# Performance work log

Measured on AMD Instinct MI355X. Metric: run time of the kernel, lower is better.

## Reference

```python
import jax, jax.numpy as jnp
import numpy as np

ENC_DIM = 512
QUERY_DIM = 1024
ATTN_DIM = 128
CONV_CH = 32
KERNEL = 31
B, T = 64, 2048


def setup_inputs() -> dict:
    key = jax.random.key(0)
    ks = jax.random.split(key, 9)
    s = 0.02
    encoder_outputs = jax.random.normal(ks[0], (B, T, ENC_DIM), dtype=jnp.float32)
    decoder_hidden = jax.random.normal(ks[1], (B, QUERY_DIM), dtype=jnp.float32)
    prev_attention = jax.random.uniform(ks[2], (B, T), dtype=jnp.float32)
    prev_attention = prev_attention / jnp.sum(prev_attention, axis=1, keepdims=True)
    Wq = jax.random.normal(ks[3], (QUERY_DIM, ATTN_DIM), dtype=jnp.float32) * s
    Wk = jax.random.normal(ks[4], (ENC_DIM, ATTN_DIM), dtype=jnp.float32) * s
    conv_w = jax.random.normal(ks[5], (CONV_CH, 1, KERNEL), dtype=jnp.float32) * s  # OIH
    conv_b = jax.random.normal(ks[6], (CONV_CH,), dtype=jnp.float32) * s
    Wloc = jax.random.normal(ks[7], (CONV_CH, ATTN_DIM), dtype=jnp.float32) * s
    v = jax.random.normal(ks[8], (ATTN_DIM,), dtype=jnp.float32) * s
    return {"encoder_outputs": encoder_outputs, "decoder_hidden": decoder_hidden,
            "prev_attention": prev_attention, "Wq": Wq, "Wk": Wk,
            "conv_w": conv_w, "conv_b": conv_b, "Wloc": Wloc, "v": v}


def reference(encoder_outputs, decoder_hidden, prev_attention, Wq, Wk, conv_w, conv_b, Wloc, v):
    # query: [B, 1, A]
    query = (decoder_hidden @ Wq)[:, None, :]
    # keys: [B, T, A]
    keys = jnp.einsum('bte,ea->bta', encoder_outputs, Wk)
    # location conv: prev_attention [B, T] -> [B, 1, T] -> [B, C, T], SAME padding
    pad = (KERNEL - 1) // 2
    loc = jax.lax.conv_general_dilated(
        prev_attention[:, None, :], conv_w,
        window_strides=(1,), padding=[(pad, pad)],
        dimension_numbers=('NCH', 'OIH', 'NCH'))
    loc = loc + conv_b[None, :, None]
    # [B, T, C] -> [B, T, A]
    location_term = jnp.einsum('bct,ca->bta', loc, Wloc)
    energy = jnp.einsum('bta,a->bt', jnp.tanh(keys + query + location_term), v)
    return jax.nn.softmax(energy, axis=1)
```

## Files before the change

### kernel.cpp

```cpp
#include <hip/hip_runtime.h>
#include <hip/hip_bf16.h>

#define B_  64
#define T_  2048
#define E_  512
#define Q_  1024
#define A_  128
#define C_  32
#define KW_ 31

using bf16x8 = __attribute__((ext_vector_type(8))) short;
using f32x4  = __attribute__((ext_vector_type(4))) float;

__device__ __forceinline__ short f2bf(float f) {
  union { float f; unsigned u; } x; x.f = f;
  unsigned r = x.u + 0x7fffu + ((x.u >> 16) & 1u);
  return (short)(r >> 16);
}

__device__ __forceinline__ bf16x8 pack8(float4 a, float4 b) {
  union { bf16x8 v; __hip_bfloat162 h[4]; } u;
  u.h[0] = __float22bfloat162_rn(make_float2(a.x, a.y));
  u.h[1] = __float22bfloat162_rn(make_float2(a.z, a.w));
  u.h[2] = __float22bfloat162_rn(make_float2(b.x, b.y));
  u.h[3] = __float22bfloat162_rn(make_float2(b.z, b.w));
  return u.v;
}

__device__ __forceinline__ float fast_tanh(float x) {
  float e2 = __expf(2.f * x);
  return 1.f - 2.f * __builtin_amdgcn_rcpf(e2 + 1.f);
}

__device__ __forceinline__ void gload16(const void* g, void* l) {
  __builtin_amdgcn_global_load_lds(
      (const __attribute__((address_space(1))) unsigned int*)g,
      (__attribute__((address_space(3))) unsigned int*)l, 16, 0, 0);
}

__global__ __launch_bounds__(256) void prep_kernel(
    const float* __restrict__ dh, const float* __restrict__ Wq,
    const float* __restrict__ conv_b, const float* __restrict__ Wloc,
    const float* __restrict__ Wk, const float* __restrict__ conv_w,
    unsigned short* __restrict__ wkf, float* __restrict__ q2p)
{
  int blk = blockIdx.x;
  int tid = threadIdx.x;
  if (blk < 512) {
    __shared__ float part[128];
    int b = blk >> 3, kq = blk & 7;
    int a = tid & 127, kh = tid >> 7;
    const float* dhr = dh + b * Q_ + kq * 128 + kh * 64;
    const float* wq  = Wq + (size_t)(kq * 128 + kh * 64) * A_ + a;
    float s = 0.f;
    #pragma unroll 8
    for (int k = 0; k < 64; ++k) s += dhr[k] * wq[(size_t)k * A_];
    if (kh) part[a] = s;
    __syncthreads();
    if (!kh) {
      s += part[a];
      if (kq == 0) {
        float t = 0.f;
        for (int c = 0; c < C_; ++c) t += conv_b[c] * Wloc[c * A_ + a];
        s += t;
      }
      q2p[(kq * B_ + b) * A_ + a] = s;
    }
  } else if (blk < 544) {
    int wave = tid >> 6, lane = tid & 63;
    int g = (blk - 512) * 4 + wave;
    int ks = g >> 3, nt = g & 7;
    int lg = lane >> 4, lr = lane & 15;
    bf16x8 o;
    #pragma unroll
    for (int j = 0; j < 8; ++j)
      o[j] = f2bf(Wk[(ks * 32 + lg * 8 + j) * A_ + nt * 16 + lr]);
    *(bf16x8*)(wkf + ((size_t)g * 64 + lane) * 8) = o;
  } else {
    __shared__ float G[32][128];
    for (int i = tid; i < 4096; i += 256) {
      int j = i >> 7, a = i & 127;
      float s = 0.f;
      if (j < KW_)
        for (int c = 0; c < C_; ++c) s += conv_w[c * KW_ + j] * Wloc[c * A_ + a];
      G[j][a] = s;
    }
    __syncthreads();
    int wave = tid >> 6, lane = tid & 63;
    int lg = lane >> 4, lr = lane & 15;
    #pragma unroll
    for (int h = 0; h < 2; ++h) {
      int nt = wave * 2 + h;
      bf16x8 o;
      #pragma unroll
      for (int j = 0; j < 8; ++j) o[j] = f2bf(G[lg * 8 + j][nt * 16 + lr]);
      *(bf16x8*)(wkf + ((size_t)(128 + nt) * 64 + lane) * 8) = o;
    }
  }
}

__global__ __launch_bounds__(512, 2) void energy_kernel(
    const float* __restrict__ enc, const float* __restrict__ prev,
    const unsigned short* __restrict__ wkfall,
    const float* __restrict__ q2p, const float* __restrict__ vvec,
    float* __restrict__ outexp, float* __restrict__ psum)
{
  __shared__ unsigned short sWB[69632];
  __shared__ float swsum[8];

  int tid = threadIdx.x;
  int wave = tid >> 6, lane = tid & 63;
  int lg = lane >> 4, lr = lane & 15;
  int m0 = blockIdx.x * 512;
  int b  = m0 >> 11;
  int wm = m0 + wave * 64;

  #pragma unroll
  for (int s = 0; s < 17; ++s)
    gload16(wkfall + (size_t)s * 4096 + wave * 512 + lane * 8,
            &sWB[s * 4096 + wave * 512]);

  const float* prevb = prev + b * T_;
  int tl = (m0 & (T_ - 1)) + wave * 64 + lr;
  float pv[32];
  #pragma unroll
  for (int g = 0; g < 4; ++g) {
    #pragma unroll
    for (int j = 0; j < 8; ++j) {
      int u = tl + 16 * g - 15 + lg * 8 + j;
      int uc = min(max(u, 0), T_ - 1);
      pv[g * 8 + j] = prevb[uc];
    }
  }

  const float* eR = enc + (size_t)(wm + lr) * E_ + lg * 8;
  float4 sA[8], sB[8];
  #pragma unroll
  for (int g = 0; g < 4; ++g) {
    const float* rg = eR + (size_t)g * 16 * E_;
    sA[2 * g]     = *(const float4*)(rg);
    sA[2 * g + 1] = *(const float4*)(rg + 4);
    sB[2 * g]     = *(const float4*)(rg + 32);
    sB[2 * g + 1] = *(const float4*)(rg + 36);
  }

  asm volatile("s_waitcnt vmcnt(0)" ::: "memory");
  __builtin_amdgcn_sched_barrier(0);
  __builtin_amdgcn_s_barrier();

  f32x4 acc[4][8];
  {
    bf16x8 ap[4];
    #pragma unroll
    for (int g = 0; g < 4; ++g) {
      float m[8];
      #pragma unroll
      for (int j = 0; j < 8; ++j) {
        int u = tl + 16 * g - 15 + lg * 8 + j;
        m[j] = ((unsigned)u < (unsigned)T_) ? pv[g * 8 + j] : 0.f;
      }
      ap[g] = pack8(make_float4(m[0], m[1], m[2], m[3]),
                    make_float4(m[4], m[5], m[6], m[7]));
    }
    const unsigned short* base = &sWB[16 * 4096 + lane * 8];
    #pragma unroll
    for (int nt = 0; nt < 8; ++nt) {
      bf16x8 bfr = *(const bf16x8*)(base + nt * 512);
      #pragma unroll
      for (int g = 0; g < 4; ++g)
        acc[g][nt] = __builtin_amdgcn_mfma_f32_16x16x32_bf16(ap[g], bfr, (f32x4){0,0,0,0}, 0, 0, 0);
    }
  }

  #pragma unroll 1
  for (int i = 0; i < 8; ++i) {
    {
      bf16x8 af[4];
      #pragma unroll
      for (int g = 0; g < 4; ++g) af[g] = pack8(sA[2 * g], sA[2 * g + 1]);
      if (i < 7) {
        #pragma unroll
        for (int g = 0; g < 4; ++g) {
          const float* rg = eR + (size_t)g * 16 * E_ + (2 * i + 2) * 32;
          sA[2 * g]     = *(const float4*)(rg);
          sA[2 * g + 1] = *(const float4*)(rg + 4);
        }
      }
      const unsigned short* base = &sWB[(2 * i) * 4096 + lane * 8];
      #pragma unroll
      for (int nt = 0; nt < 8; ++nt) {
        bf16x8 bfr = *(const bf16x8*)(base + nt * 512);
        #pragma unroll
        for (int g = 0; g < 4; ++g)
          acc[g][nt] = __builtin_amdgcn_mfma_f32_16x16x32_bf16(af[g], bfr, acc[g][nt], 0, 0, 0);
      }
    }
    {
      bf16x8 af[4];
      #pragma unroll
      for (int g = 0; g < 4; ++g) af[g] = pack8(sB[2 * g], sB[2 * g + 1]);
      if (i < 7) {
        #pragma unroll
        for (int g = 0; g < 4; ++g) {
          const float* rg = eR + (size_t)g * 16 * E_ + (2 * i + 3) * 32;
          sB[2 * g]     = *(const float4*)(rg);
          sB[2 * g + 1] = *(const float4*)(rg + 4);
        }
      }
      const unsigned short* base = &sWB[(2 * i + 1) * 4096 + lane * 8];
      #pragma unroll
      for (int nt = 0; nt < 8; ++nt) {
        bf16x8 bfr = *(const bf16x8*)(base + nt * 512);
        #pragma unroll
        for (int g = 0; g < 4; ++g)
          acc[g][nt] = __builtin_amdgcn_mfma_f32_16x16x32_bf16(af[g], bfr, acc[g][nt], 0, 0, 0);
      }
    }
  }

  float qv[8], vv[8];
  #pragma unroll
  for (int nt = 0; nt < 8; ++nt) {
    int n = nt * 16 + lr;
    float s = 0.f;
    #pragma unroll
    for (int p = 0; p < 8; ++p) s += q2p[(p * B_ + b) * A_ + n];
    qv[nt] = s;
    vv[nt] = vvec[n];
  }
  float ssum = 0.f;
  #pragma unroll
  for (int g = 0; g < 4; ++g) {
    float p0 = 0, p1 = 0, p2 = 0, p3 = 0;
    #pragma unroll
    for (int nt = 0; nt < 8; ++nt) {
      p0 += fast_tanh(acc[g][nt][0] + qv[nt]) * vv[nt];
      p1 += fast_tanh(acc[g][nt][1] + qv[nt]) * vv[nt];
      p2 += fast_tanh(acc[g][nt][2] + qv[nt]) * vv[nt];
      p3 += fast_tanh(acc[g][nt][3] + qv[nt]) * vv[nt];
    }
    #pragma unroll
    for (int off = 1; off < 16; off <<= 1) {
      p0 += __shfl_xor(p0, off, 64);
      p1 += __shfl_xor(p1, off, 64);
      p2 += __shfl_xor(p2, off, 64);
      p3 += __shfl_xor(p3, off, 64);
    }
    float e0 = __expf(p0), e1 = __expf(p1), e2 = __expf(p2), e3 = __expf(p3);
    ssum += (e0 + e1) + (e2 + e3);
    if (lr == 0)
      *(float4*)(outexp + wm + g * 16 + lg * 4) = make_float4(e0, e1, e2, e3);
  }
  ssum += __shfl_xor(ssum, 16, 64);
  ssum += __shfl_xor(ssum, 32, 64);
  if (lane == 0) swsum[wave] = ssum;
  __syncthreads();
  if (tid == 0) {
    float s = 0.f;
    #pragma unroll
    for (int wv = 0; wv < 8; ++wv) s += swsum[wv];
    psum[b * 4 + (blockIdx.x & 3)] = s;
  }
}

__global__ __launch_bounds__(256) void norm_kernel(float* __restrict__ out,
                                                   const float* __restrict__ psum)
{
  int b = blockIdx.x, tid = threadIdx.x;
  float s = 0.f;
  #pragma unroll
  for (int p = 0; p < 4; ++p) s += psum[b * 4 + p];
  float inv = 1.f / s;
  float4* row = (float4*)(out + (size_t)b * T_);
  #pragma unroll
  for (int j = 0; j < 2; ++j) {
    float4 x = row[tid + j * 256];
    x.x *= inv; x.y *= inv; x.z *= inv; x.w *= inv;
    row[tid + j * 256] = x;
  }
}

extern "C" void kernel_launch(void* const* d_in, const int* in_sizes, int n_in,
                              void* d_out, int out_size, void* d_ws, size_t ws_size,
                              hipStream_t stream)
{
  const float* enc   = (const float*)d_in[0];
  const float* dh    = (const float*)d_in[1];
  const float* prev  = (const float*)d_in[2];
  const float* Wq    = (const float*)d_in[3];
  const float* Wk    = (const float*)d_in[4];
  const float* convw = (const float*)d_in[5];
  const float* convb = (const float*)d_in[6];
  const float* Wloc  = (const float*)d_in[7];
  const float* v     = (const float*)d_in[8];
  float* out = (float*)d_out;

  char* w = (char*)d_ws;
  unsigned short* wkf  = (unsigned short*)w;
  float*          q2p  = (float*)(w + 139264);
  float*          psum = (float*)(w + 401408);

  hipLaunchKernelGGL(prep_kernel, dim3(545), dim3(256), 0, stream,
                     dh, Wq, convb, Wloc, Wk, convw, wkf, q2p);
  hipLaunchKernelGGL(energy_kernel, dim3(256), dim3(512), 0, stream,
                     enc, prev, wkf, q2p, v, out, psum);
  hipLaunchKernelGGL(norm_kernel, dim3(64), dim3(256), 0, stream, out, psum);
}
```

Measured before the change: 69.71 us.

## Fuse softmax normalization into energy kernel via last-block counter; stream encoder loads

Removes the separate normalization kernel. Each energy block publishes its partial exp-sum and increments a per-batch atomic counter, and the last of the four blocks for a batch row rescales the whole row in place. The prep kernel zeroes the counters, and the finishing block resets its own. Encoder-output loads now use nontemporal loads to reduce cache pollution from the large streamed tensor. This saves a kernel launch and a pass over the output, at the cost of atomics, extra fences and a tail of serialized work in the last block.

```diff
diff --git a/kernel.cpp b/kernel.cpp
--- a/kernel.cpp
+++ b/kernel.cpp
@@ -18,12 +18,12 @@
   return (short)(r >> 16);
 }
 
-__device__ __forceinline__ bf16x8 pack8(float4 a, float4 b) {
+__device__ __forceinline__ bf16x8 pack8(f32x4 a, f32x4 b) {
   union { bf16x8 v; __hip_bfloat162 h[4]; } u;
-  u.h[0] = __float22bfloat162_rn(make_float2(a.x, a.y));
-  u.h[1] = __float22bfloat162_rn(make_float2(a.z, a.w));
-  u.h[2] = __float22bfloat162_rn(make_float2(b.x, b.y));
-  u.h[3] = __float22bfloat162_rn(make_float2(b.z, b.w));
+  u.h[0] = __float22bfloat162_rn(make_float2(a[0], a[1]));
+  u.h[1] = __float22bfloat162_rn(make_float2(a[2], a[3]));
+  u.h[2] = __float22bfloat162_rn(make_float2(b[0], b[1]));
+  u.h[3] = __float22bfloat162_rn(make_float2(b[2], b[3]));
   return u.v;
 }
 
@@ -38,11 +38,16 @@
       (__attribute__((address_space(3))) unsigned int*)l, 16, 0, 0);
 }
 
+__device__ __forceinline__ f32x4 ntload4(const float* p) {
+  return __builtin_nontemporal_load((const f32x4*)p);
+}
+
 __global__ __launch_bounds__(256) void prep_kernel(
     const float* __restrict__ dh, const float* __restrict__ Wq,
     const float* __restrict__ conv_b, const float* __restrict__ Wloc,
     const float* __restrict__ Wk, const float* __restrict__ conv_w,
-    unsigned short* __restrict__ wkf, float* __restrict__ q2p)
+    unsigned short* __restrict__ wkf, float* __restrict__ q2p,
+    int* __restrict__ cnt)
 {
   int blk = blockIdx.x;
   int tid = threadIdx.x;
@@ -77,6 +82,7 @@
       o[j] = f2bf(Wk[(ks * 32 + lg * 8 + j) * A_ + nt * 16 + lr]);
     *(bf16x8*)(wkf + ((size_t)g * 64 + lane) * 8) = o;
   } else {
+    if (tid < B_) cnt[tid] = 0;
     __shared__ float G[32][128];
     for (int i = tid; i < 4096; i += 256) {
       int j = i >> 7, a = i & 127;
@@ -103,10 +109,11 @@
     const float* __restrict__ enc, const float* __restrict__ prev,
     const unsigned short* __restrict__ wkfall,
     const float* __restrict__ q2p, const float* __restrict__ vvec,
-    float* __restrict__ outexp, float* __restrict__ psum)
+    float* __restrict__ outexp, float* __restrict__ psum, int* __restrict__ cnt)
 {
   __shared__ unsigned short sWB[69632];
   __shared__ float swsum[8];
+  __shared__ int sdone;
 
   int tid = threadIdx.x;
   int wave = tid >> 6, lane = tid & 63;
@@ -134,14 +141,14 @@
   }
 
   const float* eR = enc + (size_t)(wm + lr) * E_ + lg * 8;
-  float4 sA[8], sB[8];
+  f32x4 sA[8], sB[8];
   #pragma unroll
   for (int g = 0; g < 4; ++g) {
     const float* rg = eR + (size_t)g * 16 * E_;
-    sA[2 * g]     = *(const float4*)(rg);
-    sA[2 * g + 1] = *(const float4*)(rg + 4);
-    sB[2 * g]     = *(const float4*)(rg + 32);
-    sB[2 * g + 1] = *(const float4*)(rg + 36);
+    sA[2 * g]     = ntload4(rg);
+    sA[2 * g + 1] = ntload4(rg + 4);
+    sB[2 * g]     = ntload4(rg + 32);
+    sB[2 * g + 1] = ntload4(rg + 36);
   }
 
   asm volatile("s_waitcnt vmcnt(0)" ::: "memory");
@@ -159,8 +166,9 @@
         int u = tl + 16 * g - 15 + lg * 8 + j;
         m[j] = ((unsigned)u < (unsigned)T_) ? pv[g * 8 + j] : 0.f;
       }
-      ap[g] = pack8(make_float4(m[0], m[1], m[2], m[3]),
-                    make_float4(m[4], m[5], m[6], m[7]));
+      f32x4 lo = {m[0], m[1], m[2], m[3]};
+      f32x4 hi = {m[4], m[5], m[6], m[7]};
+      ap[g] = pack8(lo, hi);
     }
     const unsigned short* base = &sWB[16 * 4096 + lane * 8];
     #pragma unroll
@@ -182,8 +190,8 @@
         #pragma unroll
         for (int g = 0; g < 4; ++g) {
           const float* rg = eR + (size_t)g * 16 * E_ + (2 * i + 2) * 32;
-          sA[2 * g]     = *(const float4*)(rg);
-          sA[2 * g + 1] = *(const float4*)(rg + 4);
+          sA[2 * g]     = ntload4(rg);
+          sA[2 * g + 1] = ntload4(rg + 4);
         }
       }
       const unsigned short* base = &sWB[(2 * i) * 4096 + lane * 8];
@@ -203,8 +211,8 @@
         #pragma unroll
         for (int g = 0; g < 4; ++g) {
           const float* rg = eR + (size_t)g * 16 * E_ + (2 * i + 3) * 32;
-          sB[2 * g]     = *(const float4*)(rg);
-          sB[2 * g + 1] = *(const float4*)(rg + 4);
+          sB[2 * g]     = ntload4(rg);
+          sB[2 * g + 1] = ntload4(rg + 4);
         }
       }
       const unsigned short* base = &sWB[(2 * i + 1) * 4096 + lane * 8];
@@ -260,23 +268,20 @@
     #pragma unroll
     for (int wv = 0; wv < 8; ++wv) s += swsum[wv];
     psum[b * 4 + (blockIdx.x & 3)] = s;
-  }
-}
-
-__global__ __launch_bounds__(256) void norm_kernel(float* __restrict__ out,
-                                                   const float* __restrict__ psum)
-{
-  int b = blockIdx.x, tid = threadIdx.x;
-  float s = 0.f;
-  #pragma unroll
-  for (int p = 0; p < 4; ++p) s += psum[b * 4 + p];
-  float inv = 1.f / s;
-  float4* row = (float4*)(out + (size_t)b * T_);
-  #pragma unroll
-  for (int j = 0; j < 2; ++j) {
-    float4 x = row[tid + j * 256];
+    __threadfence();
+    sdone = (atomicAdd(&cnt[b], 1) == 3);
+  }
+  __syncthreads();
+
+  if (sdone) {
+    __threadfence();
+    float s = psum[b * 4 + 0] + psum[b * 4 + 1] + psum[b * 4 + 2] + psum[b * 4 + 3];
+    float inv = 1.f / s;
+    float4* row = (float4*)(outexp + (size_t)b * T_);
+    float4 x = row[tid];
     x.x *= inv; x.y *= inv; x.z *= inv; x.w *= inv;
-    row[tid + j * 256] = x;
+    row[tid] = x;
+    if (tid == 0) atomicExch(&cnt[b], 0);
   }
 }
 
@@ -299,10 +304,10 @@
   unsigned short* wkf  = (unsigned short*)w;
   float*          q2p  = (float*)(w + 139264);
   float*          psum = (float*)(w + 401408);
+  int*            cnt  = (int*)(w + 402432);
 
   hipLaunchKernelGGL(prep_kernel, dim3(545), dim3(256), 0, stream,
-                     dh, Wq, convb, Wloc, Wk, convw, wkf, q2p);
+                     dh, Wq, convb, Wloc, Wk, convw, wkf, q2p, cnt);
   hipLaunchKernelGGL(energy_kernel, dim3(256), dim3(512), 0, stream,
-                     enc, prev, wkf, q2p, v, out, psum);
-  hipLaunchKernelGGL(norm_kernel, dim3(64), dim3(256), 0, stream, out, psum);
-}
+                     enc, prev, wkf, q2p, v, out, psum, cnt);
+}
```

Result: slower. 96.45 us (+38.4%).

## Restructure GEMM loop into per-row-group phases to shrink prefetch register footprint

Applied to the files above, without the earlier changes.

The main MFMA loop now processes one 16-row group at a time, covering the full K dimension for each group in turn, instead of interleaving all four groups per K step. Only two float4 pairs of encoder prefetch are held in registers rather than sixteen, which frees VGPRs and may improve occupancy or avoid spills. In exchange, each LDS B fragment is now reloaded four times, once per group, and each K step issues fewer MFMAs, so less independent work is available to hide load latency.

```diff
diff --git a/kernel.cpp b/kernel.cpp
--- a/kernel.cpp
+++ b/kernel.cpp
@@ -18,12 +18,12 @@
   return (short)(r >> 16);
 }
 
-__device__ __forceinline__ bf16x8 pack8(float4 a, float4 b) {
+__device__ __forceinline__ bf16x8 pack8(f32x4 a, f32x4 b) {
   union { bf16x8 v; __hip_bfloat162 h[4]; } u;
-  u.h[0] = __float22bfloat162_rn(make_float2(a.x, a.y));
-  u.h[1] = __float22bfloat162_rn(make_float2(a.z, a.w));
-  u.h[2] = __float22bfloat162_rn(make_float2(b.x, b.y));
-  u.h[3] = __float22bfloat162_rn(make_float2(b.z, b.w));
+  u.h[0] = __float22bfloat162_rn(make_float2(a[0], a[1]));
+  u.h[1] = __float22bfloat162_rn(make_float2(a[2], a[3]));
+  u.h[2] = __float22bfloat162_rn(make_float2(b[0], b[1]));
+  u.h[3] = __float22bfloat162_rn(make_float2(b[2], b[3]));
   return u.v;
 }
 
@@ -36,6 +36,10 @@
   __builtin_amdgcn_global_load_lds(
       (const __attribute__((address_space(1))) unsigned int*)g,
       (__attribute__((address_space(3))) unsigned int*)l, 16, 0, 0);
+}
+
+__device__ __forceinline__ f32x4 ld4(const float* p) {
+  return *(const f32x4*)p;
 }
 
 __global__ __launch_bounds__(256) void prep_kernel(
@@ -133,16 +137,12 @@
     }
   }
 
-  const float* eR = enc + (size_t)(wm + lr) * E_ + lg * 8;
-  float4 sA[8], sB[8];
-  #pragma unroll
-  for (int g = 0; g < 4; ++g) {
-    const float* rg = eR + (size_t)g * 16 * E_;
-    sA[2 * g]     = *(const float4*)(rg);
-    sA[2 * g + 1] = *(const float4*)(rg + 4);
-    sB[2 * g]     = *(const float4*)(rg + 32);
-    sB[2 * g + 1] = *(const float4*)(rg + 36);
-  }
+  const float* pb0 = enc + (size_t)(wm + lr) * E_ + lg * 8;
+  const float* pb1 = pb0 + 16 * E_;
+  const float* pb2 = pb1 + 16 * E_;
+  const float* pb3 = pb2 + 16 * E_;
+  f32x4 pA0 = ld4(pb0),      pA1 = ld4(pb0 + 4);
+  f32x4 pB0 = ld4(pb0 + 32), pB1 = ld4(pb0 + 36);
 
   asm volatile("s_waitcnt vmcnt(0)" ::: "memory");
   __builtin_amdgcn_sched_barrier(0);
@@ -159,8 +159,9 @@
         int u = tl + 16 * g - 15 + lg * 8 + j;
         m[j] = ((unsigned)u < (unsigned)T_) ? pv[g * 8 + j] : 0.f;
       }
-      ap[g] = pack8(make_float4(m[0], m[1], m[2], m[3]),
-                    make_float4(m[4], m[5], m[6], m[7]));
+      f32x4 lo = {m[0], m[1], m[2], m[3]};
+      f32x4 hi = {m[4], m[5], m[6], m[7]};
+      ap[g] = pack8(lo, hi);
     }
     const unsigned short* base = &sWB[16 * 4096 + lane * 8];
     #pragma unroll
@@ -172,51 +173,38 @@
     }
   }
 
-  #pragma unroll 1
-  for (int i = 0; i < 8; ++i) {
-    {
-      bf16x8 af[4];
-      #pragma unroll
-      for (int g = 0; g < 4; ++g) af[g] = pack8(sA[2 * g], sA[2 * g + 1]);
-      if (i < 7) {
-        #pragma unroll
-        for (int g = 0; g < 4; ++g) {
-          const float* rg = eR + (size_t)g * 16 * E_ + (2 * i + 2) * 32;
-          sA[2 * g]     = *(const float4*)(rg);
-          sA[2 * g + 1] = *(const float4*)(rg + 4);
-        }
-      }
-      const unsigned short* base = &sWB[(2 * i) * 4096 + lane * 8];
-      #pragma unroll
-      for (int nt = 0; nt < 8; ++nt) {
-        bf16x8 bfr = *(const bf16x8*)(base + nt * 512);
-        #pragma unroll
-        for (int g = 0; g < 4; ++g)
-          acc[g][nt] = __builtin_amdgcn_mfma_f32_16x16x32_bf16(af[g], bfr, acc[g][nt], 0, 0, 0);
-      }
-    }
-    {
-      bf16x8 af[4];
-      #pragma unroll
-      for (int g = 0; g < 4; ++g) af[g] = pack8(sB[2 * g], sB[2 * g + 1]);
-      if (i < 7) {
-        #pragma unroll
-        for (int g = 0; g < 4; ++g) {
-          const float* rg = eR + (size_t)g * 16 * E_ + (2 * i + 3) * 32;
-          sB[2 * g]     = *(const float4*)(rg);
-          sB[2 * g + 1] = *(const float4*)(rg + 4);
-        }
-      }
-      const unsigned short* base = &sWB[(2 * i + 1) * 4096 + lane * 8];
-      #pragma unroll
-      for (int nt = 0; nt < 8; ++nt) {
-        bf16x8 bfr = *(const bf16x8*)(base + nt * 512);
-        #pragma unroll
-        for (int g = 0; g < 4; ++g)
-          acc[g][nt] = __builtin_amdgcn_mfma_f32_16x16x32_bf16(af[g], bfr, acc[g][nt], 0, 0, 0);
-      }
-    }
-  }
+  #define PHASE(G, PB, PBN, LAST)                                              \
+    _Pragma("unroll 1")                                                        \
+    for (int k2 = 0; k2 < 8; ++k2) {                                           \
+      {                                                                        \
+        bf16x8 af = pack8(pA0, pA1);                                           \
+        const float* np = (k2 < 7) ? (PB) + (2 * k2 + 2) * 32 : (PBN);         \
+        if (!(LAST) || k2 < 7) { pA0 = ld4(np); pA1 = ld4(np + 4); }           \
+        const unsigned short* base = &sWB[(2 * k2) * 4096 + lane * 8];         \
+        _Pragma("unroll")                                                      \
+        for (int nt = 0; nt < 8; ++nt) {                                       \
+          bf16x8 bfr = *(const bf16x8*)(base + nt * 512);                      \
+          acc[G][nt] = __builtin_amdgcn_mfma_f32_16x16x32_bf16(af, bfr, acc[G][nt], 0, 0, 0); \
+        }                                                                      \
+      }                                                                        \
+      {                                                                        \
+        bf16x8 af = pack8(pB0, pB1);                                           \
+        const float* np = (k2 < 7) ? (PB) + (2 * k2 + 3) * 32 : (PBN) + 32;    \
+        if (!(LAST) || k2 < 7) { pB0 = ld4(np); pB1 = ld4(np + 4); }           \
+        const unsigned short* base = &sWB[(2 * k2 + 1) * 4096 + lane * 8];     \
+        _Pragma("unroll")                                                      \
+        for (int nt = 0; nt < 8; ++nt) {                                       \
+          bf16x8 bfr = *(const bf16x8*)(base + nt * 512);                      \
+          acc[G][nt] = __builtin_amdgcn_mfma_f32_16x16x32_bf16(af, bfr, acc[G][nt], 0, 0, 0); \
+        }                                                                      \
+      }                                                                        \
+    }
+
+  PHASE(0, pb0, pb1, false)
+  PHASE(1, pb1, pb2, false)
+  PHASE(2, pb2, pb3, false)
+  PHASE(3, pb3, pb3, true)
+  #undef PHASE
 
   float qv[8], vv[8];
   #pragma unroll
```

Result: no change. 69.43 us (-0.4%).
